# Performance work log

Hardware: AMD Instinct MI355X
Metric: run time of the kernel (lower is better)

The kernel has to match this reference:

```python
import jax, jax.numpy as jnp
import numpy as np

N = 8192  # must be divisible by 4
C = 2048


def setup_inputs() -> dict:
    key = jax.random.key(0)
    k1, k2 = jax.random.split(key, 2)
    x = jax.random.normal(k1, (N, C), dtype=jnp.float32)
    att_w = jax.random.normal(k2, (1, C), dtype=jnp.float32) * 0.02  # nn.Linear(2048,1) weight
    att_b = jnp.zeros((1,), dtype=jnp.float32)                        # nn.Linear bias
    return {"x": x, "att_w": att_w, "att_b": att_b}


def reference(x, att_w, att_b):
    n, c = x.shape
    s = n // 4  # stride
    # attention scores [N,1], split into 4 segments and normalize per segment
    w = x @ att_w.T + att_b                      # [N,1]
    w = w.reshape(4, s, 1)
    w = w / w.sum(axis=1, keepdims=True)         # per-segment normalization
    # attention-pooled centers: sum over each segment -> [4, C]
    centers = (x.reshape(4, s, c) * w).sum(axis=1)
    x_new = jnp.concatenate([x, centers], axis=0)  # [N+4, C]

    # build adjacency: identity, center block all-ones, segment<->center links
    adj = jnp.eye(n + 4, dtype=x.dtype)
    adj = adj.at[n:, n:].set(1.0)
    for i in range(4):
        adj = adj.at[i * s:(i + 1) * s, n + i].set(1.0)
        adj = adj.at[n + i, i * s:(i + 1) * s].set(1.0)

    # gen_adj: D = deg^-1/2 ; adj_out = (A @ diag(D)).T @ diag(D) = D * A^T * D
    d = adj.sum(axis=1) ** -0.5                  # [N+4]
    adj = (adj * d[None, :]).T * d[None, :]      # degree normalization as broadcast scale
    return x_new, adj
```

## Files before the change

kernel.cpp:

```cpp
#include <hip/hip_runtime.h>

constexpr int N = 8192;
constexpr int C = 2048;
constexpr int ND = N + 4;
constexpr unsigned ADJ_CHUNKS = ND / 4;
constexpr unsigned TOTAL4 = (unsigned)ND * ADJ_CHUNKS;
constexpr size_t XNEW_ELEMS = (size_t)ND * C;

#define C_DIAG 0.5f
#define C_LINK 0.015609764f
#define C_BLK  (1.0f / 2052.0f)

__global__ __launch_bounds__(256) void k_adj(float* __restrict__ adj) {
    const unsigned stride = gridDim.x * 256u;
    float4* __restrict__ out = reinterpret_cast<float4*>(adj);
    for (unsigned i4 = blockIdx.x * 256u + threadIdx.x; i4 < TOTAL4; i4 += stride) {
        const unsigned row   = i4 / ADJ_CHUNKS;
        const unsigned chunk = i4 - row * ADJ_CHUNKS;
        float4 v = make_float4(0.f, 0.f, 0.f, 0.f);
        if (row < (unsigned)N) {
            if (chunk == (row >> 2))      (&v.x)[row & 3]  = C_DIAG;
            else if (chunk == 2048u)      (&v.x)[row >> 11] = C_LINK;
        } else {
            const unsigned a = row - N;
            if (chunk == 2048u)           v = make_float4(C_BLK, C_BLK, C_BLK, C_BLK);
            else if ((chunk >> 9) == a)   v = make_float4(C_LINK, C_LINK, C_LINK, C_LINK);
        }
        out[i4] = v;
    }
}

template <bool USE_WS>
__global__ __launch_bounds__(256) void k_att(const float* __restrict__ x,
                                             const float* __restrict__ attw,
                                             const float* __restrict__ attb,
                                             float* __restrict__ xnew,
                                             float* __restrict__ part,
                                             float* __restrict__ wpart) {
    __shared__ float lnum[4][C];
    __shared__ float lw[4];

    const int tid  = threadIdx.x;
    const int wave = tid >> 6;
    const int lane = tid & 63;
    const int row0 = blockIdx.x * 16;
    const int seg  = blockIdx.x >> 7;
    const float bias = attb[0];

    float4 wv[8];
#pragma unroll
    for (int q = 0; q < 8; ++q)
        wv[q] = reinterpret_cast<const float4*>(attw)[lane + 64 * q];

    float acc[32];
#pragma unroll
    for (int k = 0; k < 32; ++k) acc[k] = 0.0f;
    float wacc = 0.0f;

    for (int r = 0; r < 4; ++r) {
        const int row = row0 + wave * 4 + r;
        const float4* xrow = reinterpret_cast<const float4*>(x + (size_t)row * C);
        float4* orow = reinterpret_cast<float4*>(xnew + (size_t)row * C);

        float4 xv[8];
        float dot = 0.0f;
#pragma unroll
        for (int q = 0; q < 8; ++q) {
            xv[q] = xrow[lane + 64 * q];
            dot += xv[q].x * wv[q].x + xv[q].y * wv[q].y +
                   xv[q].z * wv[q].z + xv[q].w * wv[q].w;
        }
#pragma unroll
        for (int off = 32; off > 0; off >>= 1) dot += __shfl_xor(dot, off, 64);
        const float wrow = dot + bias;
        wacc += wrow;
#pragma unroll
        for (int q = 0; q < 8; ++q) {
            acc[4 * q + 0] += wrow * xv[q].x;
            acc[4 * q + 1] += wrow * xv[q].y;
            acc[4 * q + 2] += wrow * xv[q].z;
            acc[4 * q + 3] += wrow * xv[q].w;
            orow[lane + 64 * q] = xv[q];
        }
    }

#pragma unroll
    for (int q = 0; q < 8; ++q)
        reinterpret_cast<float4*>(&lnum[wave][0])[lane + 64 * q] =
            make_float4(acc[4 * q], acc[4 * q + 1], acc[4 * q + 2], acc[4 * q + 3]);
    if (lane == 0) lw[wave] = wacc;
    __syncthreads();

    const float4* l0 = reinterpret_cast<const float4*>(&lnum[0][0]);
    const float4* l1 = reinterpret_cast<const float4*>(&lnum[1][0]);
    const float4* l2 = reinterpret_cast<const float4*>(&lnum[2][0]);
    const float4* l3 = reinterpret_cast<const float4*>(&lnum[3][0]);
#pragma unroll
    for (int c4 = tid; c4 < C / 4; c4 += 256) {
        float4 a = l0[c4], b = l1[c4], cc = l2[c4], d = l3[c4];
        float4 s = make_float4(a.x + b.x + cc.x + d.x, a.y + b.y + cc.y + d.y,
                               a.z + b.z + cc.z + d.z, a.w + b.w + cc.w + d.w);
        if constexpr (USE_WS) {
            reinterpret_cast<float4*>(part + (size_t)blockIdx.x * C)[c4] = s;
        } else {
            float* dst = &xnew[(size_t)(N + seg) * C + 4 * c4];
            atomicAdd(dst + 0, s.x); atomicAdd(dst + 1, s.y);
            atomicAdd(dst + 2, s.z); atomicAdd(dst + 3, s.w);
        }
    }
    if (tid == 0) {
        const float wb = lw[0] + lw[1] + lw[2] + lw[3];
        if constexpr (USE_WS) wpart[blockIdx.x] = wb;
        else                  atomicAdd(&wpart[seg], wb);
    }
}

__global__ __launch_bounds__(256) void k_centers(const float* __restrict__ part,
                                                 const float* __restrict__ wpart,
                                                 float* __restrict__ xnew) {
    const int idx = blockIdx.x * 256 + threadIdx.x;
    const int seg = idx >> 11;
    const int c   = idx & 2047;
    float wsum = 0.0f;
#pragma unroll 8
    for (int k = 0; k < 128; ++k) wsum += wpart[seg * 128 + k];
    float s = 0.0f;
#pragma unroll 8
    for (int k = 0; k < 128; ++k) s += part[(size_t)(seg * 128 + k) * C + c];
    xnew[(size_t)(N + seg) * C + c] = s / wsum;
}

__global__ __launch_bounds__(256) void k_zero(float* __restrict__ xnew,
                                              float* __restrict__ wseg) {
    int idx = blockIdx.x * 256 + threadIdx.x;
    if (idx < 4 * C) xnew[(size_t)N * C + idx] = 0.0f;
    if (idx < 4) wseg[idx] = 0.0f;
}
__global__ __launch_bounds__(256) void k_div(float* __restrict__ xnew,
                                             const float* __restrict__ wseg) {
    int idx = blockIdx.x * 256 + threadIdx.x;
    if (idx < 4 * C) xnew[(size_t)N * C + idx] /= wseg[idx >> 11];
}

extern "C" void kernel_launch(void* const* d_in, const int* in_sizes, int n_in,
                              void* d_out, int out_size, void* d_ws, size_t ws_size,
                              hipStream_t stream) {
    const float* x    = (const float*)d_in[0];
    const float* attw = (const float*)d_in[1];
    const float* attb = (const float*)d_in[2];
    float* xnew = (float*)d_out;
    float* adj  = (float*)d_out + XNEW_ELEMS;

    const size_t ws_need = (1024 + (size_t)512 * C) * sizeof(float);
    if (ws_size >= ws_need) {
        float* wpart = (float*)d_ws;
        float* part  = (float*)d_ws + 1024;
        k_att<true><<<N / 16, 256, 0, stream>>>(x, attw, attb, xnew, part, wpart);
        k_centers<<<32, 256, 0, stream>>>(part, wpart, xnew);
    } else {
        float* wseg = (float*)d_ws;
        k_zero<<<32, 256, 0, stream>>>(xnew, wseg);
        k_att<false><<<N / 16, 256, 0, stream>>>(x, attw, attb, xnew, nullptr, wseg);
        k_div<<<32, 256, 0, stream>>>(xnew, wseg);
    }

    k_adj<<<2048, 256, 0, stream>>>(adj);
}
```

Before: 113.2 us.

## Fuse attention-pooling and adjacency fill into one launch with nontemporal stores

Merges the attention-pooling kernel and the adjacency-matrix fill into a single heterogeneous grid, where the first blocks do pooling and the rest write adj, so the two memory-bound phases overlap and one launch is saved. Pooling blocks drop the LDS cross-wave reduction and __syncthreads, writing per-wave partials instead. This quadruples the partials k_centers must sum, so that reduction does more traffic. Loads and stores use nontemporal hints, and the adj fill becomes branch-free selects.

```diff
diff --git a/kernel.cpp b/kernel.cpp
--- a/kernel.cpp
+++ b/kernel.cpp
@@ -6,112 +6,104 @@
 constexpr unsigned ADJ_CHUNKS = ND / 4;
 constexpr unsigned TOTAL4 = (unsigned)ND * ADJ_CHUNKS;
 constexpr size_t XNEW_ELEMS = (size_t)ND * C;
+constexpr int ATT_BLOCKS = 512;
+constexpr int ADJ_BLOCKS = 2048;
 
 #define C_DIAG 0.5f
 #define C_LINK 0.015609764f
 #define C_BLK  (1.0f / 2052.0f)
 
-__global__ __launch_bounds__(256) void k_adj(float* __restrict__ adj) {
-    const unsigned stride = gridDim.x * 256u;
-    float4* __restrict__ out = reinterpret_cast<float4*>(adj);
-    for (unsigned i4 = blockIdx.x * 256u + threadIdx.x; i4 < TOTAL4; i4 += stride) {
+typedef float f32x4 __attribute__((ext_vector_type(4)));
+
+__device__ __forceinline__ void adj_body(float* __restrict__ adj,
+                                         unsigned first, unsigned stride) {
+    f32x4* __restrict__ out = reinterpret_cast<f32x4*>(adj);
+    for (unsigned i4 = first; i4 < TOTAL4; i4 += stride) {
         const unsigned row   = i4 / ADJ_CHUNKS;
         const unsigned chunk = i4 - row * ADJ_CHUNKS;
-        float4 v = make_float4(0.f, 0.f, 0.f, 0.f);
+        f32x4 v;
         if (row < (unsigned)N) {
-            if (chunk == (row >> 2))      (&v.x)[row & 3]  = C_DIAG;
-            else if (chunk == 2048u)      (&v.x)[row >> 11] = C_LINK;
+            const bool dg = (chunk == (row >> 2));
+            const bool lk = (chunk == 2048u);
+            const unsigned r3 = row & 3u, sg = row >> 11;
+            v.x = (dg && r3 == 0u) ? C_DIAG : ((lk && sg == 0u) ? C_LINK : 0.0f);
+            v.y = (dg && r3 == 1u) ? C_DIAG : ((lk && sg == 1u) ? C_LINK : 0.0f);
+            v.z = (dg && r3 == 2u) ? C_DIAG : ((lk && sg == 2u) ? C_LINK : 0.0f);
+            v.w = (dg && r3 == 3u) ? C_DIAG : ((lk && sg == 3u) ? C_LINK : 0.0f);
         } else {
             const unsigned a = row - N;
-            if (chunk == 2048u)           v = make_float4(C_BLK, C_BLK, C_BLK, C_BLK);
-            else if ((chunk >> 9) == a)   v = make_float4(C_LINK, C_LINK, C_LINK, C_LINK);
-        }
-        out[i4] = v;
-    }
-}
-
-template <bool USE_WS>
-__global__ __launch_bounds__(256) void k_att(const float* __restrict__ x,
-                                             const float* __restrict__ attw,
-                                             const float* __restrict__ attb,
-                                             float* __restrict__ xnew,
-                                             float* __restrict__ part,
-                                             float* __restrict__ wpart) {
-    __shared__ float lnum[4][C];
-    __shared__ float lw[4];
-
-    const int tid  = threadIdx.x;
-    const int wave = tid >> 6;
-    const int lane = tid & 63;
-    const int row0 = blockIdx.x * 16;
-    const int seg  = blockIdx.x >> 7;
-    const float bias = attb[0];
-
-    float4 wv[8];
-#pragma unroll
-    for (int q = 0; q < 8; ++q)
-        wv[q] = reinterpret_cast<const float4*>(attw)[lane + 64 * q];
-
-    float acc[32];
-#pragma unroll
-    for (int k = 0; k < 32; ++k) acc[k] = 0.0f;
-    float wacc = 0.0f;
-
-    for (int r = 0; r < 4; ++r) {
-        const int row = row0 + wave * 4 + r;
-        const float4* xrow = reinterpret_cast<const float4*>(x + (size_t)row * C);
-        float4* orow = reinterpret_cast<float4*>(xnew + (size_t)row * C);
-
-        float4 xv[8];
-        float dot = 0.0f;
+            const float f = (chunk == 2048u) ? C_BLK
+                          : (((chunk >> 9) == a) ? C_LINK : 0.0f);
+            v.x = f; v.y = f; v.z = f; v.w = f;
+        }
+        __builtin_nontemporal_store(v, &out[i4]);
+    }
+}
+
+__global__ __launch_bounds__(256) void k_fused(const float* __restrict__ x,
+                                               const float* __restrict__ attw,
+                                               const float* __restrict__ attb,
+                                               float* __restrict__ xnew,
+                                               float* __restrict__ adj,
+                                               float* __restrict__ part,
+                                               float* __restrict__ wpart) {
+    const int tid = threadIdx.x;
+    if (blockIdx.x < ATT_BLOCKS) {
+        const int wave = tid >> 6;
+        const int lane = tid & 63;
+        const int row0 = blockIdx.x * 16;
+        const float bias = attb[0];
+
+        f32x4 wv[8];
+#pragma unroll
+        for (int q = 0; q < 8; ++q)
+            wv[q] = reinterpret_cast<const f32x4*>(attw)[lane + 64 * q];
+
+        float acc[32];
+#pragma unroll
+        for (int k = 0; k < 32; ++k) acc[k] = 0.0f;
+        float wacc = 0.0f;
+
+        for (int r = 0; r < 4; ++r) {
+            const int row = row0 + wave * 4 + r;
+            const f32x4* xrow = reinterpret_cast<const f32x4*>(x + (size_t)row * C);
+            f32x4* orow = reinterpret_cast<f32x4*>(xnew + (size_t)row * C);
+
+            f32x4 xv[8];
+            float dot = 0.0f;
+#pragma unroll
+            for (int q = 0; q < 8; ++q) {
+                xv[q] = __builtin_nontemporal_load(&xrow[lane + 64 * q]);
+                dot += xv[q].x * wv[q].x + xv[q].y * wv[q].y +
+                       xv[q].z * wv[q].z + xv[q].w * wv[q].w;
+            }
+#pragma unroll
+            for (int off = 32; off > 0; off >>= 1) dot += __shfl_xor(dot, off, 64);
+            const float wrow = dot + bias;
+            wacc += wrow;
+#pragma unroll
+            for (int q = 0; q < 8; ++q) {
+                acc[4 * q + 0] += wrow * xv[q].x;
+                acc[4 * q + 1] += wrow * xv[q].y;
+                acc[4 * q + 2] += wrow * xv[q].z;
+                acc[4 * q + 3] += wrow * xv[q].w;
+                __builtin_nontemporal_store(xv[q], &orow[lane + 64 * q]);
+            }
+        }
+
+        const int gw = blockIdx.x * 4 + wave;
+        f32x4* prow = reinterpret_cast<f32x4*>(part + (size_t)gw * C);
 #pragma unroll
         for (int q = 0; q < 8; ++q) {
-            xv[q] = xrow[lane + 64 * q];
-            dot += xv[q].x * wv[q].x + xv[q].y * wv[q].y +
-                   xv[q].z * wv[q].z + xv[q].w * wv[q].w;
-        }
-#pragma unroll
-        for (int off = 32; off > 0; off >>= 1) dot += __shfl_xor(dot, off, 64);
-        const float wrow = dot + bias;
-        wacc += wrow;
-#pragma unroll
-        for (int q = 0; q < 8; ++q) {
-            acc[4 * q + 0] += wrow * xv[q].x;
-            acc[4 * q + 1] += wrow * xv[q].y;
-            acc[4 * q + 2] += wrow * xv[q].z;
-            acc[4 * q + 3] += wrow * xv[q].w;
-            orow[lane + 64 * q] = xv[q];
-        }
-    }
-
-#pragma unroll
-    for (int q = 0; q < 8; ++q)
-        reinterpret_cast<float4*>(&lnum[wave][0])[lane + 64 * q] =
-            make_float4(acc[4 * q], acc[4 * q + 1], acc[4 * q + 2], acc[4 * q + 3]);
-    if (lane == 0) lw[wave] = wacc;
-    __syncthreads();
-
-    const float4* l0 = reinterpret_cast<const float4*>(&lnum[0][0]);
-    const float4* l1 = reinterpret_cast<const float4*>(&lnum[1][0]);
-    const float4* l2 = reinterpret_cast<const float4*>(&lnum[2][0]);
-    const float4* l3 = reinterpret_cast<const float4*>(&lnum[3][0]);
-#pragma unroll
-    for (int c4 = tid; c4 < C / 4; c4 += 256) {
-        float4 a = l0[c4], b = l1[c4], cc = l2[c4], d = l3[c4];
-        float4 s = make_float4(a.x + b.x + cc.x + d.x, a.y + b.y + cc.y + d.y,
-                               a.z + b.z + cc.z + d.z, a.w + b.w + cc.w + d.w);
-        if constexpr (USE_WS) {
-            reinterpret_cast<float4*>(part + (size_t)blockIdx.x * C)[c4] = s;
-        } else {
-            float* dst = &xnew[(size_t)(N + seg) * C + 4 * c4];
-            atomicAdd(dst + 0, s.x); atomicAdd(dst + 1, s.y);
-            atomicAdd(dst + 2, s.z); atomicAdd(dst + 3, s.w);
-        }
-    }
-    if (tid == 0) {
-        const float wb = lw[0] + lw[1] + lw[2] + lw[3];
-        if constexpr (USE_WS) wpart[blockIdx.x] = wb;
-        else                  atomicAdd(&wpart[seg], wb);
+            f32x4 s;
+            s.x = acc[4 * q];     s.y = acc[4 * q + 1];
+            s.z = acc[4 * q + 2]; s.w = acc[4 * q + 3];
+            prow[lane + 64 * q] = s;
+        }
+        if (lane == 0) wpart[gw] = wacc;
+    } else {
+        adj_body(adj, (blockIdx.x - ATT_BLOCKS) * 256u + (unsigned)tid,
+                 ADJ_BLOCKS * 256u);
     }
 }
 
@@ -123,18 +115,79 @@
     const int c   = idx & 2047;
     float wsum = 0.0f;
 #pragma unroll 8
-    for (int k = 0; k < 128; ++k) wsum += wpart[seg * 128 + k];
+    for (int k = 0; k < 512; ++k) wsum += wpart[seg * 512 + k];
     float s = 0.0f;
 #pragma unroll 8
-    for (int k = 0; k < 128; ++k) s += part[(size_t)(seg * 128 + k) * C + c];
+    for (int k = 0; k < 512; ++k) s += part[(size_t)(seg * 512 + k) * C + c];
     xnew[(size_t)(N + seg) * C + c] = s / wsum;
 }
 
+__global__ __launch_bounds__(256) void k_adj_only(float* __restrict__ adj) {
+    adj_body(adj, blockIdx.x * 256u + (unsigned)threadIdx.x, ADJ_BLOCKS * 256u);
+}
 __global__ __launch_bounds__(256) void k_zero(float* __restrict__ xnew,
                                               float* __restrict__ wseg) {
     int idx = blockIdx.x * 256 + threadIdx.x;
     if (idx < 4 * C) xnew[(size_t)N * C + idx] = 0.0f;
     if (idx < 4) wseg[idx] = 0.0f;
+}
+__global__ __launch_bounds__(256) void k_att_atomic(const float* __restrict__ x,
+                                                    const float* __restrict__ attw,
+                                                    const float* __restrict__ attb,
+                                                    float* __restrict__ xnew,
+                                                    float* __restrict__ wseg) {
+    __shared__ float lnum[4][C];
+    __shared__ float lw[4];
+    const int tid = threadIdx.x, wave = tid >> 6, lane = tid & 63;
+    const int row0 = blockIdx.x * 16, seg = blockIdx.x >> 7;
+    const float bias = attb[0];
+    f32x4 wv[8];
+#pragma unroll
+    for (int q = 0; q < 8; ++q)
+        wv[q] = reinterpret_cast<const f32x4*>(attw)[lane + 64 * q];
+    float acc[32];
+#pragma unroll
+    for (int k = 0; k < 32; ++k) acc[k] = 0.0f;
+    float wacc = 0.0f;
+    for (int r = 0; r < 4; ++r) {
+        const int row = row0 + wave * 4 + r;
+        const f32x4* xrow = reinterpret_cast<const f32x4*>(x + (size_t)row * C);
+        f32x4* orow = reinterpret_cast<f32x4*>(xnew + (size_t)row * C);
+        f32x4 xv[8];
+        float dot = 0.0f;
+#pragma unroll
+        for (int q = 0; q < 8; ++q) {
+            xv[q] = xrow[lane + 64 * q];
+            dot += xv[q].x * wv[q].x + xv[q].y * wv[q].y +
+                   xv[q].z * wv[q].z + xv[q].w * wv[q].w;
+        }
+#pragma unroll
+        for (int off = 32; off > 0; off >>= 1) dot += __shfl_xor(dot, off, 64);
+        const float wrow = dot + bias;
+        wacc += wrow;
+#pragma unroll
+        for (int q = 0; q < 8; ++q) {
+            acc[4 * q + 0] += wrow * xv[q].x;
+            acc[4 * q + 1] += wrow * xv[q].y;
+            acc[4 * q + 2] += wrow * xv[q].z;
+            acc[4 * q + 3] += wrow * xv[q].w;
+            orow[lane + 64 * q] = xv[q];
+        }
+    }
+#pragma unroll
+    for (int q = 0; q < 8; ++q) {
+        f32x4 s;
+        s.x = acc[4 * q];     s.y = acc[4 * q + 1];
+        s.z = acc[4 * q + 2]; s.w = acc[4 * q + 3];
+        reinterpret_cast<f32x4*>(&lnum[wave][0])[lane + 64 * q] = s;
+    }
+    if (lane == 0) lw[wave] = wacc;
+    __syncthreads();
+    for (int c = tid; c < C; c += 256) {
+        float s = lnum[0][c] + lnum[1][c] + lnum[2][c] + lnum[3][c];
+        atomicAdd(&xnew[(size_t)(N + seg) * C + c], s);
+    }
+    if (tid == 0) atomicAdd(&wseg[seg], lw[0] + lw[1] + lw[2] + lw[3]);
 }
 __global__ __launch_bounds__(256) void k_div(float* __restrict__ xnew,
                                              const float* __restrict__ wseg) {
@@ -151,18 +204,18 @@
     float* xnew = (float*)d_out;
     float* adj  = (float*)d_out + XNEW_ELEMS;
 
-    const size_t ws_need = (1024 + (size_t)512 * C) * sizeof(float);
+    const size_t ws_need = (2048 + (size_t)2048 * C) * sizeof(float);
     if (ws_size >= ws_need) {
         float* wpart = (float*)d_ws;
-        float* part  = (float*)d_ws + 1024;
-        k_att<true><<<N / 16, 256, 0, stream>>>(x, attw, attb, xnew, part, wpart);
+        float* part  = (float*)d_ws + 2048;
+        k_fused<<<ATT_BLOCKS + ADJ_BLOCKS, 256, 0, stream>>>(
+            x, attw, attb, xnew, adj, part, wpart);
         k_centers<<<32, 256, 0, stream>>>(part, wpart, xnew);
     } else {
         float* wseg = (float*)d_ws;
         k_zero<<<32, 256, 0, stream>>>(xnew, wseg);
-        k_att<false><<<N / 16, 256, 0, stream>>>(x, attw, attb, xnew, nullptr, wseg);
+        k_att_atomic<<<N / 16, 256, 0, stream>>>(x, attw, attb, xnew, wseg);
         k_div<<<32, 256, 0, stream>>>(xnew, wseg);
-    }
-
-    k_adj<<<2048, 256, 0, stream>>>(adj);
-}
+        k_adj_only<<<ADJ_BLOCKS, 256, 0, stream>>>(adj);
+    }
+}
```

Result: slower. 120.3 us (+6.3%).
